# Kernel tuning notes

Hardware: AMD Instinct MI355X
Metric: run time of the kernel (lower is better)

The kernel has to match this reference:

```python
import jax, jax.numpy as jnp
import numpy as np

B, S, D, H = 2, 2048, 1024, 16
DK = D // H

def setup_inputs() -> dict:
    key = jax.random.key(0)
    ks = jax.random.split(key, 11)
    def lin(kw, kb):
        # torch nn.Linear init scale ~ 1/sqrt(fan_in)
        s = 1.0 / np.sqrt(D)
        W = jax.random.uniform(kw, (D, D), jnp.float32, -s, s)
        b = jax.random.uniform(kb, (D,), jnp.float32, -s, s)
        return W, b
    Wq, bq = lin(ks[0], ks[1])
    Wk, bk = lin(ks[2], ks[3])
    Wv, bv = lin(ks[4], ks[5])
    Wo, bo = lin(ks[6], ks[7])
    query = jax.random.normal(ks[8], (B, S, D), jnp.float32)
    key_t = jax.random.normal(ks[9], (B, S, D), jnp.float32)
    value = jax.random.normal(ks[10], (B, S, D), jnp.float32)
    return {"query": query, "key": key_t, "value": value,
            "Wq": Wq, "bq": bq, "Wk": Wk, "bk": bk,
            "Wv": Wv, "bv": bv, "Wo": Wo, "bo": bo}

def reference(query, key, value, Wq, bq, Wk, bk, Wv, bv, Wo, bo):
    # linear projections (torch Linear: x @ W.T + b), split heads -> (B,H,S,DK)
    def proj(x, W, b):
        y = jnp.einsum('bsd,ed->bse', x, W) + b
        return y.reshape(B, -1, H, DK).transpose(0, 2, 1, 3)
    q = proj(query, Wq, bq)
    k = proj(key, Wk, bk)
    v = proj(value, Wv, bv)
    # scaled dot-product attention, full score matrix (B,H,Sq,Sk)
    scores = jnp.einsum('bhqd,bhkd->bhqk', q, k) / jnp.sqrt(jnp.float32(DK))
    attn = jax.nn.softmax(scores, axis=-1)
    ctx = jnp.einsum('bhqk,bhkd->bhqd', attn, v)
    # merge heads and output projection; dropout is identity in eval mode
    ctx = ctx.transpose(0, 2, 1, 3).reshape(B, -1, D)
    out = jnp.einsum('bsd,ed->bse', ctx, Wo) + bo
    attn_weights = attn.mean(axis=1)  # average_weights=True -> (B,Sq,Sk)
    return (out, attn_weights)
```

## Files before the change

### kernel.cpp

```cpp
#include <hip/hip_runtime.h>

#define B_ 2
#define S_ 2048
#define D_ 1024
#define H_ 16
#define DK_ 64
#define M_ (B_ * S_)

typedef __bf16 bf16;
typedef __attribute__((ext_vector_type(8))) __bf16 bf16x8;
typedef __attribute__((ext_vector_type(4))) __bf16 bf16x4;
typedef __attribute__((ext_vector_type(4))) float f32x4;

static __device__ __forceinline__ bf16x8 ld8(const bf16* p) {
    return *(const bf16x8*)p;
}

static __device__ __forceinline__ void g2l16(const void* g, void* l) {
    __builtin_amdgcn_global_load_lds(
        (const __attribute__((address_space(1))) unsigned int*)g,
        (__attribute__((address_space(3))) unsigned int*)l, 16, 0, 0);
}

__global__ __launch_bounds__(256)
void cvt_all(const float* __restrict__ xq, const float* __restrict__ xk,
             const float* __restrict__ xv, const float* __restrict__ wq,
             const float* __restrict__ wk, const float* __restrict__ wv,
             const float* __restrict__ wo, bf16* __restrict__ xqo,
             bf16* __restrict__ xko, bf16* __restrict__ xvo,
             bf16* __restrict__ wqo, bf16* __restrict__ wko,
             bf16* __restrict__ wvo, bf16* __restrict__ woo)
{
    const int bx = blockIdx.x;
    const float* s; bf16* d; size_t base;
    if (bx < 6144) {
        int a = bx >> 11;
        s = (a == 0) ? xq : (a == 1) ? xk : xv;
        d = (a == 0) ? xqo : (a == 1) ? xko : xvo;
        base = (size_t)(bx & 2047) * 2048;
    } else {
        int a = (bx - 6144) >> 9;
        s = (a == 0) ? wq : (a == 1) ? wk : (a == 2) ? wv : wo;
        d = (a == 0) ? wqo : (a == 1) ? wko : (a == 2) ? wvo : woo;
        base = (size_t)((bx - 6144) & 511) * 2048;
    }
    size_t i = base + (size_t)threadIdx.x * 8;
    f32x4 a4 = *(const f32x4*)(s + i);
    f32x4 b4 = *(const f32x4*)(s + i + 4);
    bf16x8 r;
    r[0]=(bf16)a4[0]; r[1]=(bf16)a4[1]; r[2]=(bf16)a4[2]; r[3]=(bf16)a4[3];
    r[4]=(bf16)b4[0]; r[5]=(bf16)b4[1]; r[6]=(bf16)b4[2]; r[7]=(bf16)b4[3];
    *(bf16x8*)(d + i) = r;
}

__global__ __launch_bounds__(256)
void gemm128(const bf16* __restrict__ A, const bf16* __restrict__ W,
             const float* __restrict__ bias, void* __restrict__ out,
             int a_headsplit, int out_mode, float scale)
{
    const int m0 = blockIdx.x * 128, n0 = blockIdx.y * 128;
    const int tid = threadIdx.x;
    const int wv = tid >> 6, lane = tid & 63, quad = lane >> 4, l16 = lane & 15;
    const int wr = (wv >> 1) * 64, wc = (wv & 1) * 64;

    __shared__ bf16 As[128 * 32];
    __shared__ bf16 Bs[128 * 32];

    f32x4 acc[4][4];
#pragma unroll
    for (int i = 0; i < 4; ++i)
#pragma unroll
        for (int j = 0; j < 4; ++j) acc[i][j] = f32x4{0.f, 0.f, 0.f, 0.f};

    const int srow = tid >> 2;
    const int scol = (tid & 3) * 8;

    for (int k0 = 0; k0 < D_; k0 += 32) {
        bf16x8 av[2], bw[2];
#pragma unroll
        for (int c = 0; c < 2; ++c) {
            const int row = c * 64 + srow;
            const int k   = k0 + scol;
            const bf16* ap;
            if (a_headsplit) {
                int m = m0 + row, bb = m >> 11, ss = m & (S_ - 1);
                int hh = k >> 6, dd = k & (DK_ - 1);
                ap = A + (((size_t)(bb * H_ + hh) * S_ + ss) * DK_ + dd);
            } else {
                ap = A + (size_t)(m0 + row) * D_ + k;
            }
            av[c] = ld8(ap);
            bw[c] = ld8(W + (size_t)(n0 + row) * D_ + k);
        }
        __syncthreads();
#pragma unroll
        for (int c = 0; c < 2; ++c) {
            const int e = c * 2048 + tid * 8;
            *(bf16x8*)(As + e) = av[c];
            *(bf16x8*)(Bs + e) = bw[c];
        }
        __syncthreads();

        bf16x8 af[4], bfr[4];
#pragma unroll
        for (int i = 0; i < 4; ++i)
            af[i] = *(const bf16x8*)(As + (wr + i*16 + l16) * 32 + quad * 8);
#pragma unroll
        for (int j = 0; j < 4; ++j)
            bfr[j] = *(const bf16x8*)(Bs + (wc + j*16 + l16) * 32 + quad * 8);
#pragma unroll
        for (int i = 0; i < 4; ++i)
#pragma unroll
            for (int j = 0; j < 4; ++j)
                acc[i][j] = __builtin_amdgcn_mfma_f32_16x16x32_bf16(
                    af[i], bfr[j], acc[i][j], 0, 0, 0);
    }

    if (out_mode == 2) {
#pragma unroll
        for (int j = 0; j < 4; ++j) {
            const int nn = n0 + wc + j*16 + l16;
            const float bvv = bias[nn];
            int hh = nn >> 6, dd = nn & (DK_ - 1);
#pragma unroll
            for (int ip = 0; ip < 2; ++ip) {
                const int mlo = m0 + wr + 32*ip + quad*4;
                int bb = mlo >> 11, sl = mlo & (S_ - 1);
                int g0 = (sl & ~31) + ((sl & 15) << 1);
                bf16x8 pk;
#pragma unroll
                for (int r = 0; r < 4; ++r) {
                    pk[2*r]   = (bf16)((acc[2*ip  ][j][r] + bvv) * scale);
                    pk[2*r+1] = (bf16)((acc[2*ip+1][j][r] + bvv) * scale);
                }
                *(bf16x8*)((bf16*)out +
                    ((size_t)(bb * H_ + hh) * DK_ + dd) * S_ + g0) = pk;
            }
        }
    } else {
#pragma unroll
        for (int i = 0; i < 4; ++i)
#pragma unroll
            for (int j = 0; j < 4; ++j) {
                const int nn = n0 + wc + j*16 + l16;
                const float bvv = bias[nn];
                const int mm0 = m0 + wr + i*16 + quad*4;
#pragma unroll
                for (int r = 0; r < 4; ++r) {
                    const int mm = mm0 + r;
                    float v = (acc[i][j][r] + bvv) * scale;
                    if (out_mode == 1) {
                        ((float*)out)[(size_t)mm * D_ + nn] = v;
                    } else {
                        int bb = mm >> 11, ss = mm & (S_ - 1);
                        int hh = nn >> 6, dd = nn & (DK_ - 1);
                        ((bf16*)out)[((size_t)(bb * H_ + hh) * S_ + ss) * DK_ + dd] = (bf16)v;
                    }
                }
            }
    }
}

__global__ __launch_bounds__(256)
void attn_ctx(const bf16* __restrict__ Q, const bf16* __restrict__ K,
              const bf16* __restrict__ Vt, float* __restrict__ Li,
              bf16* __restrict__ ctxOut)
{
    const int bid = blockIdx.x;
    const int l   = (bid & 7) * 128 + (bid >> 3);
    const int q0  = (l & 31) * 64;
    const int h   = (l >> 5) & 15;
    const int b   = l >> 9;

    const int tid = threadIdx.x;
    const int wv = tid >> 6, lane = tid & 63, quad = lane >> 4, l16 = lane & 15;

    __shared__ bf16 Kl[2][4096];
    __shared__ bf16 Vl[2][4096];

    const size_t hb = (size_t)(b * H_ + h) * S_;
    const int qw = q0 + wv * 16;

    bf16x8 qf0, qf1;
    {
        const bf16* qrow = Q + (hb + qw + l16) * DK_;
        qf0 = ld8(qrow + quad*8);
        qf1 = ld8(qrow + 32 + quad*8);
    }
    const char* Kbc = (const char*)(K  + hb * DK_);
    const char* Vbc = (const char*)(Vt + hb * DK_);

    f32x4 cacc[4];
#pragma unroll
    for (int db = 0; db < 4; ++db) cacc[db] = f32x4{0.f,0.f,0.f,0.f};
    float lsum = 0.f;

    const int rbK  = wv * 16;
    const int rlan = lane >> 3;
    const int off  = (((lane & 7) ^ rlan) << 4);

#define STAGE(jc, buf)                                                        \
    do {                                                                      \
        const size_t jb = (size_t)(jc) * 64;                                  \
        g2l16(Kbc + (jb + rbK + rlan) * 128 + off,      &Kl[buf][rbK*64]);    \
        g2l16(Kbc + (jb + rbK + 8 + rlan) * 128 + off,  &Kl[buf][(rbK+8)*64]);\
        g2l16(Vbc + (size_t)(rbK + rlan) * (S_*2) + jb*2 + off,               \
              &Vl[buf][rbK*64]);                                              \
        g2l16(Vbc + (size_t)(rbK + 8 + rlan) * (S_*2) + jb*2 + off,           \
              &Vl[buf][(rbK+8)*64]);                                          \
    } while (0)

    STAGE(0, 0);
    __syncthreads();

    int cur = 0;
    const int sw = (l16 & 7) << 4;
    for (int jc = 0; jc < 32; ++jc) {
        STAGE((jc + 1) & 31, cur ^ 1);

        const char* kb = (const char*)&Kl[cur][0];
        const char* vb = (const char*)&Vl[cur][0];

        f32x4 sc[4];
#pragma unroll
        for (int t = 0; t < 4; ++t) {
            const char* kr = kb + (t*16 + l16) * 128;
            bf16x8 ka = *(const bf16x8*)(kr + ((quad*16) ^ sw));
            bf16x8 kbv = *(const bf16x8*)(kr + ((64 + quad*16) ^ sw));
            f32x4 z = {0.f,0.f,0.f,0.f};
            z = __builtin_amdgcn_mfma_f32_16x16x32_bf16(ka, qf0, z, 0, 0, 0);
            sc[t] = __builtin_amdgcn_mfma_f32_16x16x32_bf16(kbv, qf1, z, 0, 0, 0);
        }

        float ex[4][4];
#pragma unroll
        for (int t = 0; t < 4; ++t)
#pragma unroll
            for (int r = 0; r < 4; ++r)
                ex[t][r] = __builtin_amdgcn_exp2f(fminf(sc[t][r], 86.f));
#pragma unroll
        for (int t = 0; t < 4; ++t)
            lsum += (ex[t][0] + ex[t][1]) + (ex[t][2] + ex[t][3]);

        bf16x8 pa0, pa1;
#pragma unroll
        for (int r = 0; r < 4; ++r) {
            pa0[2*r]   = (bf16)ex[0][r];
            pa0[2*r+1] = (bf16)ex[1][r];
            pa1[2*r]   = (bf16)ex[2][r];
            pa1[2*r+1] = (bf16)ex[3][r];
        }

#pragma unroll
        for (int db = 0; db < 4; ++db) {
            const char* vr = vb + (db*16 + l16) * 128;
            bf16x8 va0 = *(const bf16x8*)(vr + ((quad*16) ^ sw));
            bf16x8 va1 = *(const bf16x8*)(vr + ((64 + quad*16) ^ sw));
            cacc[db] = __builtin_amdgcn_mfma_f32_16x16x32_bf16(
                va0, pa0, cacc[db], 0, 0, 0);
            cacc[db] = __builtin_amdgcn_mfma_f32_16x16x32_bf16(
                va1, pa1, cacc[db], 0, 0, 0);
        }

        __syncthreads();
        cur ^= 1;
    }
#undef STAGE

    lsum += __shfl_xor(lsum, 16);
    lsum += __shfl_xor(lsum, 32);
    const float linv = 1.0f / fmaxf(lsum, 1e-30f);
    if (lane < 16) Li[hb + qw + lane] = lsum;

#pragma unroll
    for (int db = 0; db < 4; ++db) {
        bf16x4 pk;
#pragma unroll
        for (int r = 0; r < 4; ++r) pk[r] = (bf16)(cacc[db][r] * linv);
        *(bf16x4*)(ctxOut + (hb + qw + l16) * DK_ + db*16 + quad*4) = pk;
    }
}

__global__ __launch_bounds__(256)
void attn_weights(const bf16* __restrict__ Q, const bf16* __restrict__ K,
                  const float* __restrict__ Li, float* __restrict__ attnOut)
{
    const int bid = blockIdx.x;
    const int l   = (bid & 7) * 64 + (bid >> 3);
    const int q0  = (l & 31) * 64;
    const int b   = (l >> 5) & 1;
    const int j0  = (l >> 6) * 256;

    const int tid = threadIdx.x;
    const int wv = tid >> 6, lane = tid & 63, quad = lane >> 4, l16 = lane & 15;

    __shared__ float linv[H_][64];
#pragma unroll
    for (int i = 0; i < 4; ++i) {
        int idx = tid * 4 + i;
        int hh = idx >> 6, row = idx & 63;
        linv[hh][row] = (1.0f / H_) /
            fmaxf(Li[(size_t)(b * H_ + hh) * S_ + q0 + row], 1e-30f);
    }
    __syncthreads();

    f32x4 asum[4][4];
#pragma unroll
    for (int qt = 0; qt < 4; ++qt)
#pragma unroll
        for (int t = 0; t < 4; ++t) asum[qt][t] = f32x4{0.f,0.f,0.f,0.f};

    bf16x8 qc[4][2];
    {
        const size_t hb0 = (size_t)(b * H_) * S_;
#pragma unroll
        for (int qt = 0; qt < 4; ++qt) {
            const bf16* qrow = Q + (hb0 + q0 + qt*16 + l16) * DK_;
            qc[qt][0] = ld8(qrow + quad*8);
            qc[qt][1] = ld8(qrow + 32 + quad*8);
        }
    }

    for (int h = 0; h < H_; ++h) {
        const size_t hb = (size_t)(b * H_ + h) * S_;

        bf16x8 kA[4], kB[4];
#pragma unroll
        for (int t = 0; t < 4; ++t) {
            const bf16* krow = K + (hb + (size_t)(j0 + wv*64 + t*16 + l16)) * DK_;
            kA[t] = ld8(krow + quad*8);
            kB[t] = ld8(krow + 32 + quad*8);
        }

        bf16x8 qn[4][2];
        {
            const size_t hbn = (size_t)(b * H_ + ((h + 1) & 15)) * S_;
#pragma unroll
            for (int qt = 0; qt < 4; ++qt) {
                const bf16* qrow = Q + (hbn + q0 + qt*16 + l16) * DK_;
                qn[qt][0] = ld8(qrow + quad*8);
                qn[qt][1] = ld8(qrow + 32 + quad*8);
            }
        }

        float lv[4];
#pragma unroll
        for (int qt = 0; qt < 4; ++qt) lv[qt] = linv[h][qt*16 + l16];

#pragma unroll
        for (int t = 0; t < 4; ++t)
#pragma unroll
            for (int qt = 0; qt < 4; ++qt) {
                f32x4 z = {0.f,0.f,0.f,0.f};
                z = __builtin_amdgcn_mfma_f32_16x16x32_bf16(kA[t], qc[qt][0], z, 0, 0, 0);
                f32x4 s = __builtin_amdgcn_mfma_f32_16x16x32_bf16(kB[t], qc[qt][1], z, 0, 0, 0);
#pragma unroll
                for (int r = 0; r < 4; ++r)
                    asum[qt][t][r] += __builtin_amdgcn_exp2f(fminf(s[r], 86.f)) * lv[qt];
            }

#pragma unroll
        for (int qt = 0; qt < 4; ++qt) {
            qc[qt][0] = qn[qt][0];
            qc[qt][1] = qn[qt][1];
        }
    }

#pragma unroll
    for (int qt = 0; qt < 4; ++qt)
#pragma unroll
        for (int t = 0; t < 4; ++t)
            *(f32x4*)(attnOut + ((size_t)b * S_ + q0 + qt*16 + l16) * S_
                      + j0 + wv*64 + t*16 + quad*4) = asum[qt][t];
}

extern "C" void kernel_launch(void* const* d_in, const int* in_sizes, int n_in,
                              void* d_out, int out_size, void* d_ws, size_t ws_size,
                              hipStream_t stream)
{
    (void)in_sizes; (void)n_in; (void)out_size; (void)ws_size;

    const float* query = (const float*)d_in[0];
    const float* key_t = (const float*)d_in[1];
    const float* value = (const float*)d_in[2];
    const float* Wq = (const float*)d_in[3];
    const float* bq = (const float*)d_in[4];
    const float* Wk = (const float*)d_in[5];
    const float* bk = (const float*)d_in[6];
    const float* Wv = (const float*)d_in[7];
    const float* bv = (const float*)d_in[8];
    const float* Wo = (const float*)d_in[9];
    const float* bo = (const float*)d_in[10];

    float* out     = (float*)d_out;
    float* attnOut = out + (size_t)B_ * S_ * D_;

    const size_t nX = (size_t)B_ * S_ * D_;
    const size_t nW = (size_t)D_ * D_;

    bf16* Xqb = (bf16*)d_out;
    bf16* Xkb = Xqb + nX;
    bf16* Xvb = Xkb + nX;

    bf16* Qh  = (bf16*)d_ws;
    bf16* Kh  = Qh + nX;
    bf16* VtH = Kh + nX;
    bf16* Wob = VtH + nX;
    float* Li = (float*)(Wob + nW);
    bf16* Wqb = (bf16*)(Li + (size_t)B_ * H_ * S_);
    bf16* Wkb = Wqb + nW;
    bf16* Wvb = Wkb + nW;
    bf16* CtxH = Wqb;

    cvt_all<<<8192, 256, 0, stream>>>(query, key_t, value, Wq, Wk, Wv, Wo,
                                      Xqb, Xkb, Xvb, Wqb, Wkb, Wvb, Wob);
    dim3 gg(M_/128, D_/128);
    gemm128<<<gg, 256, 0, stream>>>(Xqb, Wqb, bq, Qh, 0, 0, 0.18033688011112042f);
    gemm128<<<gg, 256, 0, stream>>>(Xkb, Wkb, bk, Kh, 0, 0, 1.0f);
    gemm128<<<gg, 256, 0, stream>>>(Xvb, Wvb, bv, VtH, 0, 2, 1.0f);
    attn_ctx    <<<1024, 256, 0, stream>>>(Qh, Kh, VtH, Li, CtxH);
    attn_weights<<<512, 256, 0, stream>>>(Qh, Kh, Li, attnOut);
    gemm128<<<gg, 256, 0, stream>>>(CtxH, Wob, bo, out, 1, 1, 1.0f);
}
```

Before: 341.5 us.

## Merge QKV projections into one launch with double-buffered direct-to-LDS loads

The three Q/K/V projection GEMMs become a single 768-block launch that picks its operands from the block index. Their main loop now stages tiles with global_load_lds straight into double-buffered shared memory, so the next tile's fetch overlaps the MFMAs on the current one and each step needs one barrier instead of two. The output projection keeps a specialised copy of the old GEMM. The cost is twice the LDS per block and no padding or swizzle on the LDS layout, which may cause bank conflicts.

```diff
diff --git a/kernel.cpp b/kernel.cpp
--- a/kernel.cpp
+++ b/kernel.cpp
@@ -54,17 +54,30 @@
 }
 
 __global__ __launch_bounds__(256)
-void gemm128(const bf16* __restrict__ A, const bf16* __restrict__ W,
-             const float* __restrict__ bias, void* __restrict__ out,
-             int a_headsplit, int out_mode, float scale)
-{
-    const int m0 = blockIdx.x * 128, n0 = blockIdx.y * 128;
+void gemm_qkv(const bf16* __restrict__ Xq, const bf16* __restrict__ Xk,
+              const bf16* __restrict__ Xv, const bf16* __restrict__ Wq,
+              const bf16* __restrict__ Wk, const bf16* __restrict__ Wv,
+              const float* __restrict__ bq, const float* __restrict__ bk,
+              const float* __restrict__ bv, bf16* __restrict__ Qo,
+              bf16* __restrict__ Ko, bf16* __restrict__ Vo)
+{
+    const int bid = blockIdx.x;
+    const int which = bid >> 8;
+    const int inner = bid & 255;
+    const int m0 = (inner >> 3) * 128;
+    const int n0 = (inner & 7) * 128;
+
+    const bf16* A = (which == 0) ? Xq : (which == 1) ? Xk : Xv;
+    const bf16* W = (which == 0) ? Wq : (which == 1) ? Wk : Wv;
+    const float* bias = (which == 0) ? bq : (which == 1) ? bk : bv;
+    const float scale = (which == 0) ? 0.18033688011112042f : 1.0f;
+
     const int tid = threadIdx.x;
     const int wv = tid >> 6, lane = tid & 63, quad = lane >> 4, l16 = lane & 15;
     const int wr = (wv >> 1) * 64, wc = (wv & 1) * 64;
 
-    __shared__ bf16 As[128 * 32];
-    __shared__ bf16 Bs[128 * 32];
+    __shared__ bf16 As[2][128 * 32];
+    __shared__ bf16 Bs[2][128 * 32];
 
     f32x4 acc[4][4];
 #pragma unroll
@@ -72,51 +85,48 @@
 #pragma unroll
         for (int j = 0; j < 4; ++j) acc[i][j] = f32x4{0.f, 0.f, 0.f, 0.f};
 
-    const int srow = tid >> 2;
-    const int scol = (tid & 3) * 8;
-
-    for (int k0 = 0; k0 < D_; k0 += 32) {
-        bf16x8 av[2], bw[2];
-#pragma unroll
-        for (int c = 0; c < 2; ++c) {
-            const int row = c * 64 + srow;
-            const int k   = k0 + scol;
-            const bf16* ap;
-            if (a_headsplit) {
-                int m = m0 + row, bb = m >> 11, ss = m & (S_ - 1);
-                int hh = k >> 6, dd = k & (DK_ - 1);
-                ap = A + (((size_t)(bb * H_ + hh) * S_ + ss) * DK_ + dd);
-            } else {
-                ap = A + (size_t)(m0 + row) * D_ + k;
-            }
-            av[c] = ld8(ap);
-            bw[c] = ld8(W + (size_t)(n0 + row) * D_ + k);
-        }
-        __syncthreads();
-#pragma unroll
-        for (int c = 0; c < 2; ++c) {
-            const int e = c * 2048 + tid * 8;
-            *(bf16x8*)(As + e) = av[c];
-            *(bf16x8*)(Bs + e) = bw[c];
-        }
-        __syncthreads();
+    const int srow = lane >> 2;
+    const int sk   = (lane & 3) * 8;
+
+#define GSTAGE(k0, buf)                                                       \
+    do {                                                                      \
+        _Pragma("unroll")                                                     \
+        for (int c = 0; c < 2; ++c) {                                         \
+            const int rb = c * 64 + wv * 16;                                  \
+            g2l16(A + (size_t)(m0 + rb + srow) * D_ + (k0) + sk,              \
+                  &As[buf][rb * 32]);                                         \
+            g2l16(W + (size_t)(n0 + rb + srow) * D_ + (k0) + sk,              \
+                  &Bs[buf][rb * 32]);                                         \
+        }                                                                     \
+    } while (0)
+
+    GSTAGE(0, 0);
+    __syncthreads();
+
+    int cur = 0;
+    for (int ks = 0; ks < 32; ++ks) {
+        GSTAGE(((ks + 1) & 31) * 32, cur ^ 1);
 
         bf16x8 af[4], bfr[4];
 #pragma unroll
         for (int i = 0; i < 4; ++i)
-            af[i] = *(const bf16x8*)(As + (wr + i*16 + l16) * 32 + quad * 8);
+            af[i] = *(const bf16x8*)(&As[cur][(wr + i*16 + l16) * 32 + quad * 8]);
 #pragma unroll
         for (int j = 0; j < 4; ++j)
-            bfr[j] = *(const bf16x8*)(Bs + (wc + j*16 + l16) * 32 + quad * 8);
+            bfr[j] = *(const bf16x8*)(&Bs[cur][(wc + j*16 + l16) * 32 + quad * 8]);
 #pragma unroll
         for (int i = 0; i < 4; ++i)
 #pragma unroll
             for (int j = 0; j < 4; ++j)
                 acc[i][j] = __builtin_amdgcn_mfma_f32_16x16x32_bf16(
                     af[i], bfr[j], acc[i][j], 0, 0, 0);
-    }
-
-    if (out_mode == 2) {
+
+        __syncthreads();
+        cur ^= 1;
+    }
+#undef GSTAGE
+
+    if (which == 2) {
 #pragma unroll
         for (int j = 0; j < 4; ++j) {
             const int nn = n0 + wc + j*16 + l16;
@@ -130,14 +140,14 @@
                 bf16x8 pk;
 #pragma unroll
                 for (int r = 0; r < 4; ++r) {
-                    pk[2*r]   = (bf16)((acc[2*ip  ][j][r] + bvv) * scale);
-                    pk[2*r+1] = (bf16)((acc[2*ip+1][j][r] + bvv) * scale);
+                    pk[2*r]   = (bf16)(acc[2*ip  ][j][r] + bvv);
+                    pk[2*r+1] = (bf16)(acc[2*ip+1][j][r] + bvv);
                 }
-                *(bf16x8*)((bf16*)out +
-                    ((size_t)(bb * H_ + hh) * DK_ + dd) * S_ + g0) = pk;
+                *(bf16x8*)(Vo + ((size_t)(bb * H_ + hh) * DK_ + dd) * S_ + g0) = pk;
             }
         }
     } else {
+        bf16* out = (which == 0) ? Qo : Ko;
 #pragma unroll
         for (int i = 0; i < 4; ++i)
 #pragma unroll
@@ -145,20 +155,85 @@
                 const int nn = n0 + wc + j*16 + l16;
                 const float bvv = bias[nn];
                 const int mm0 = m0 + wr + i*16 + quad*4;
+                int hh = nn >> 6, dd = nn & (DK_ - 1);
 #pragma unroll
                 for (int r = 0; r < 4; ++r) {
                     const int mm = mm0 + r;
-                    float v = (acc[i][j][r] + bvv) * scale;
-                    if (out_mode == 1) {
-                        ((float*)out)[(size_t)mm * D_ + nn] = v;
-                    } else {
-                        int bb = mm >> 11, ss = mm & (S_ - 1);
-                        int hh = nn >> 6, dd = nn & (DK_ - 1);
-                        ((bf16*)out)[((size_t)(bb * H_ + hh) * S_ + ss) * DK_ + dd] = (bf16)v;
-                    }
+                    int bb = mm >> 11, ss = mm & (S_ - 1);
+                    out[((size_t)(bb * H_ + hh) * S_ + ss) * DK_ + dd] =
+                        (bf16)((acc[i][j][r] + bvv) * scale);
                 }
             }
     }
+}
+
+__global__ __launch_bounds__(256)
+void gemm128(const bf16* __restrict__ A, const bf16* __restrict__ W,
+             const float* __restrict__ bias, float* __restrict__ out)
+{
+    const int m0 = blockIdx.x * 128, n0 = blockIdx.y * 128;
+    const int tid = threadIdx.x;
+    const int wv = tid >> 6, lane = tid & 63, quad = lane >> 4, l16 = lane & 15;
+    const int wr = (wv >> 1) * 64, wc = (wv & 1) * 64;
+
+    __shared__ bf16 As[128 * 32];
+    __shared__ bf16 Bs[128 * 32];
+
+    f32x4 acc[4][4];
+#pragma unroll
+    for (int i = 0; i < 4; ++i)
+#pragma unroll
+        for (int j = 0; j < 4; ++j) acc[i][j] = f32x4{0.f, 0.f, 0.f, 0.f};
+
+    const int srow = tid >> 2;
+    const int scol = (tid & 3) * 8;
+
+    for (int k0 = 0; k0 < D_; k0 += 32) {
+        bf16x8 av[2], bw[2];
+#pragma unroll
+        for (int c = 0; c < 2; ++c) {
+            const int row = c * 64 + srow;
+            const int k   = k0 + scol;
+            int m = m0 + row, bb = m >> 11, ss = m & (S_ - 1);
+            int hh = k >> 6, dd = k & (DK_ - 1);
+            av[c] = ld8(A + (((size_t)(bb * H_ + hh) * S_ + ss) * DK_ + dd));
+            bw[c] = ld8(W + (size_t)(n0 + row) * D_ + k);
+        }
+        __syncthreads();
+#pragma unroll
+        for (int c = 0; c < 2; ++c) {
+            const int e = c * 2048 + tid * 8;
+            *(bf16x8*)(As + e) = av[c];
+            *(bf16x8*)(Bs + e) = bw[c];
+        }
+        __syncthreads();
+
+        bf16x8 af[4], bfr[4];
+#pragma unroll
+        for (int i = 0; i < 4; ++i)
+            af[i] = *(const bf16x8*)(As + (wr + i*16 + l16) * 32 + quad * 8);
+#pragma unroll
+        for (int j = 0; j < 4; ++j)
+            bfr[j] = *(const bf16x8*)(Bs + (wc + j*16 + l16) * 32 + quad * 8);
+#pragma unroll
+        for (int i = 0; i < 4; ++i)
+#pragma unroll
+            for (int j = 0; j < 4; ++j)
+                acc[i][j] = __builtin_amdgcn_mfma_f32_16x16x32_bf16(
+                    af[i], bfr[j], acc[i][j], 0, 0, 0);
+    }
+
+#pragma unroll
+    for (int i = 0; i < 4; ++i)
+#pragma unroll
+        for (int j = 0; j < 4; ++j) {
+            const int nn = n0 + wc + j*16 + l16;
+            const float bvv = bias[nn];
+            const int mm0 = m0 + wr + i*16 + quad*4;
+#pragma unroll
+            for (int r = 0; r < 4; ++r)
+                out[(size_t)(mm0 + r) * D_ + nn] = acc[i][j][r] + bvv;
+        }
 }
 
 __global__ __launch_bounds__(256)
@@ -414,11 +489,10 @@
 
     cvt_all<<<8192, 256, 0, stream>>>(query, key_t, value, Wq, Wk, Wv, Wo,
                                       Xqb, Xkb, Xvb, Wqb, Wkb, Wvb, Wob);
-    dim3 gg(M_/128, D_/128);
-    gemm128<<<gg, 256, 0, stream>>>(Xqb, Wqb, bq, Qh, 0, 0, 0.18033688011112042f);
-    gemm128<<<gg, 256, 0, stream>>>(Xkb, Wkb, bk, Kh, 0, 0, 1.0f);
-    gemm128<<<gg, 256, 0, stream>>>(Xvb, Wvb, bv, VtH, 0, 2, 1.0f);
+    gemm_qkv<<<768, 256, 0, stream>>>(Xqb, Xkb, Xvb, Wqb, Wkb, Wvb,
+                                      bq, bk, bv, Qh, Kh, VtH);
     attn_ctx    <<<1024, 256, 0, stream>>>(Qh, Kh, VtH, Li, CtxH);
     attn_weights<<<512, 256, 0, stream>>>(Qh, Kh, Li, attnOut);
-    gemm128<<<gg, 256, 0, stream>>>(CtxH, Wob, bo, out, 1, 1, 1.0f);
-}
+    dim3 gg(M_/128, D_/128);
+    gemm128<<<gg, 256, 0, stream>>>(CtxH, Wob, bo, out);
+}
```

New measurement: 317.3 us. 7.1% less time.
